# Kernel tuning notes

Hardware: AMD Instinct MI355X
Metric: run time of the kernel (lower is better)

Reference implementation:

```python
import jax, jax.numpy as jnp
import numpy as np

CHEB_K = 3


def setup_inputs() -> dict:
    key = jax.random.key(0)
    k1, k2, k3 = jax.random.split(key, 3)
    B, N, C = 64, 2048, 64
    E, O = 16, 64
    x = jax.random.normal(k1, (B, N, C), dtype=jnp.float32)
    node_embeddings = jax.random.normal(k2, (N, E), dtype=jnp.float32)
    # xavier-uniform-like init for weights_pool (embed_dim, cheb_k, dim_in, dim_out)
    fan_in, fan_out = E * CHEB_K * C, O
    limit = float(np.sqrt(6.0 / (fan_in + fan_out)))
    weights_pool = jax.random.uniform(k3, (E, CHEB_K, C, O), dtype=jnp.float32,
                                      minval=-limit, maxval=limit)
    bias_pool = jnp.zeros((E, O), dtype=jnp.float32)
    return {"x": x, "node_embeddings": node_embeddings,
            "weights_pool": weights_pool, "bias_pool": bias_pool}


def reference(x, node_embeddings, weights_pool, bias_pool):
    N = node_embeddings.shape[0]
    # adaptive adjacency: softmax(relu(E E^T)) row-wise   [N, N]
    supports = jax.nn.softmax(jax.nn.relu(node_embeddings @ node_embeddings.T), axis=1)
    # Chebyshev recurrence: T0 = I, T1 = A, Tk = 2*A*T_{k-1} - T_{k-2}
    support_set = [jnp.eye(N, dtype=supports.dtype), supports]
    for _ in range(2, CHEB_K):
        support_set.append(2.0 * supports @ support_set[-1] - support_set[-2])
    supports_k = jnp.stack(support_set, axis=0)  # [K, N, N]
    # per-node dynamic weights / bias from pools
    weights = jnp.einsum('nd,dkio->nkio', node_embeddings, weights_pool)  # [N,K,C,O]
    bias = node_embeddings @ bias_pool                                    # [N,O]
    # graph conv: gather Chebyshev features then per-node grouped GEMM
    x_g = jnp.einsum('knm,bmc->bnkc', supports_k, x)       # [B,N,K,C]
    x_gconv = jnp.einsum('bnki,nkio->bno', x_g, weights) + bias  # [B,N,O]
    return x_gconv
```

## Files before the change

kernel.cpp:

```cpp
#include <hip/hip_runtime.h>
#include <hip/hip_bf16.h>

#define BB 64
#define NN 2048
#define CC 64
#define EE 16
#define OO 64
#define JJ 4096

typedef __attribute__((ext_vector_type(8))) short short8;
typedef __attribute__((ext_vector_type(4))) float f32x4;
typedef __attribute__((ext_vector_type(4))) unsigned short u16x4;
typedef __attribute__((ext_vector_type(8))) unsigned short u16x8;

__device__ __forceinline__ unsigned short f2bf(float f) {
  __hip_bfloat16 h = __float2bfloat16(f);
  return *reinterpret_cast<unsigned short*>(&h);
}
__device__ __forceinline__ float bf2f(unsigned short u) {
  unsigned int v = ((unsigned int)u) << 16;
  return *reinterpret_cast<float*>(&v);
}
__device__ __forceinline__ void gload16(const void* g, void* l) {
  __builtin_amdgcn_global_load_lds(
      (const __attribute__((address_space(1))) unsigned int*)g,
      (__attribute__((address_space(3))) unsigned int*)l, 16, 0, 0);
}

__global__ __launch_bounds__(256) void supports_kernel(
    const float* __restrict__ emb, unsigned short* __restrict__ A)
{
  int n = blockIdx.x;
  int tid = threadIdx.x;
  float en[EE];
#pragma unroll
  for (int d = 0; d < EE; ++d) en[d] = emb[n*EE + d];

  float logit[8];
  float lmax = 0.0f;
#pragma unroll
  for (int i = 0; i < 8; ++i) {
    int m = i*256 + tid;
    const float* em = emb + m*EE;
    float s = 0.f;
#pragma unroll
    for (int d = 0; d < EE; ++d) s = fmaf(en[d], em[d], s);
    s = fmaxf(s, 0.f);
    logit[i] = s;
    lmax = fmaxf(lmax, s);
  }
  __shared__ float red[256];
  red[tid] = lmax; __syncthreads();
  for (int s = 128; s > 0; s >>= 1) {
    if (tid < s) red[tid] = fmaxf(red[tid], red[tid+s]);
    __syncthreads();
  }
  lmax = red[0]; __syncthreads();
  float sum = 0.f;
#pragma unroll
  for (int i = 0; i < 8; ++i) {
    float e = __expf(logit[i]-lmax);
    logit[i] = e; sum += e;
  }
  red[tid] = sum; __syncthreads();
  for (int s = 128; s > 0; s >>= 1) {
    if (tid < s) red[tid] += red[tid+s];
    __syncthreads();
  }
  float inv = 1.f/red[0];
#pragma unroll
  for (int i = 0; i < 8; ++i) A[(size_t)n*NN + i*256 + tid] = f2bf(logit[i]*inv);
}

__global__ __launch_bounds__(256) void xpose_kernel(
    const float* __restrict__ x, unsigned short* __restrict__ Xt)
{
  int b = blockIdx.y;
  int n0 = blockIdx.x * 64;
  __shared__ float T[64][65];
  int tid = threadIdx.x;
  int r = tid >> 4, c4 = (tid & 15) * 4;
  const float* src = x + ((size_t)b*NN + n0)*64;
#pragma unroll
  for (int rr = r; rr < 64; rr += 16) {
    float4 v = *(const float4*)(src + rr*64 + c4);
    T[rr][c4] = v.x; T[rr][c4+1] = v.y; T[rr][c4+2] = v.z; T[rr][c4+3] = v.w;
  }
  __syncthreads();
  int c = tid >> 2, q0 = (tid & 3) * 16;
  unsigned short* dst = Xt + ((size_t)b*64 + c)*NN + n0 + q0;
  u16x8 o0, o1;
#pragma unroll
  for (int q = 0; q < 8; ++q) o0[q] = f2bf(T[q0+q][c]);
#pragma unroll
  for (int q = 0; q < 8; ++q) o1[q] = f2bf(T[q0+8+q][c]);
  *(u16x8*)(dst) = o0;
  *(u16x8*)(dst + 8) = o1;
}

#define BAR() do { asm volatile("" ::: "memory"); __builtin_amdgcn_s_barrier(); \
                   asm volatile("" ::: "memory"); } while(0)

__global__ __launch_bounds__(512) void gemm_bt_8p(
    const unsigned short* __restrict__ A, const unsigned short* __restrict__ Bt,
    unsigned short* __restrict__ Crow, unsigned short* __restrict__ Ct, int writeT)
{
  __shared__ unsigned short As[3][128*64];
  __shared__ unsigned short Bs[3][256*64];
  int tid = threadIdx.x;
  int bid = blockIdx.x;
  int swz = (bid & 7) * 32 + (bid >> 3);
  int m0 = (swz >> 4) * 128, j0 = (swz & 15) * 256;
  int wid = tid >> 6, lane = tid & 63;
  int wm = wid >> 2, wn = wid & 3;
  int fr = lane & 15, kg = lane >> 4;
  int lrow = lane >> 3, lu = lane & 7;

  f32x4 acc[4][4];
#pragma unroll
  for (int i = 0; i < 4; ++i)
#pragma unroll
    for (int j = 0; j < 4; ++j) acc[i][j] = (f32x4){0.f,0.f,0.f,0.f};

  auto stageA = [&](int bW, int k0, int c) {
    int rb = wid*16 + c*8;
    gload16(A + (size_t)(m0 + rb + lrow)*2048 + k0 + (lu ^ lrow)*8, &As[bW][rb*64]);
  };
  auto stageB = [&](int bW, int k0, int c) {
    int rb = wid*32 + c*8;
    gload16(Bt + (size_t)(j0 + rb + lrow)*2048 + k0 + (lu ^ lrow)*8, &Bs[bW][rb*64]);
  };
  auto phase = [&](int bR, int q) {
    int qi = q >> 1, qj = q & 1;
    short8 af[2][2], bv[2][2];
#pragma unroll
    for (int di = 0; di < 2; ++di)
#pragma unroll
      for (int ks = 0; ks < 2; ++ks) {
        int r = wm*64 + (qi*2 + di)*16 + fr;
        int u = ((ks << 2) | kg) ^ (r & 7);
        af[di][ks] = *(const short8*)((const char*)&As[bR][0] + r*128 + u*16);
      }
#pragma unroll
    for (int dj = 0; dj < 2; ++dj)
#pragma unroll
      for (int ks = 0; ks < 2; ++ks) {
        int r = wn*64 + (qj*2 + dj)*16 + fr;
        int u = ((ks << 2) | kg) ^ (r & 7);
        bv[dj][ks] = *(const short8*)((const char*)&Bs[bR][0] + r*128 + u*16);
      }
    __builtin_amdgcn_s_setprio(1);
#pragma unroll
    for (int di = 0; di < 2; ++di)
#pragma unroll
      for (int dj = 0; dj < 2; ++dj)
#pragma unroll
        for (int ks = 0; ks < 2; ++ks)
          acc[qi*2+di][qj*2+dj] = __builtin_amdgcn_mfma_f32_16x16x32_bf16(
              af[di][ks], bv[dj][ks], acc[qi*2+di][qj*2+dj], 0, 0, 0);
    __builtin_amdgcn_s_setprio(0);
  };

#define TILE(bR, bW, kS, DOST, EW) do {                                   \
    if (DOST) { stageA(bW, kS, 0); stageB(bW, kS, 0); }                   \
    phase(bR, 0); BAR();                                                  \
    if (DOST) { stageA(bW, kS, 1); stageB(bW, kS, 1); }                   \
    phase(bR, 1); BAR();                                                  \
    if (DOST) { stageB(bW, kS, 2); stageB(bW, kS, 3); }                   \
    phase(bR, 2); BAR();                                                  \
    phase(bR, 3);                                                         \
    if ((EW) == 6) asm volatile("s_waitcnt vmcnt(6)" ::: "memory");       \
    else if ((EW) == 0) asm volatile("s_waitcnt vmcnt(0)" ::: "memory");  \
    if ((EW) >= 0) BAR();                                                 \
  } while(0)

  stageA(0, 0, 0); stageA(0, 0, 1);
  stageB(0, 0, 0); stageB(0, 0, 1); stageB(0, 0, 2); stageB(0, 0, 3);
  stageA(1, 64, 0); stageA(1, 64, 1);
  stageB(1, 64, 0); stageB(1, 64, 1); stageB(1, 64, 2); stageB(1, 64, 3);
  asm volatile("s_waitcnt vmcnt(6)" ::: "memory");
  BAR();

  for (int tg = 0; tg < 10; ++tg) {
    int kb = tg * 192;
    TILE(0, 2, kb + 128, 1, 6);
    TILE(1, 0, kb + 192, 1, 6);
    TILE(2, 1, kb + 256, 1, 6);
  }
  TILE(0, 2, 0, 0, 0);
  TILE(1, 0, 0, 0, -1);
#undef TILE

  int mrow4 = (lane >> 4) * 4;
#pragma unroll
  for (int i = 0; i < 4; ++i) {
    int mbase = m0 + wm*64 + i*16 + mrow4;
#pragma unroll
    for (int j = 0; j < 4; ++j) {
      int jcol = j0 + wn*64 + j*16 + fr;
      f32x4 v = acc[i][j];
      if (writeT) {
        u16x4 pk = { f2bf(v[0]), f2bf(v[1]), f2bf(v[2]), f2bf(v[3]) };
        *(u16x4*)(Ct + (size_t)jcol*2048 + mbase) = pk;
      }
      Crow[(size_t)(mbase+0)*4096 + jcol] = f2bf(v[0]);
      Crow[(size_t)(mbase+1)*4096 + jcol] = f2bf(v[1]);
      Crow[(size_t)(mbase+2)*4096 + jcol] = f2bf(v[2]);
      Crow[(size_t)(mbase+3)*4096 + jcol] = f2bf(v[3]);
    }
  }
}

__global__ __launch_bounds__(256) void wgen_kernel(
    const float* __restrict__ emb, const float* __restrict__ wp,
    unsigned short* __restrict__ wtg)
{
  __shared__ unsigned short Wlds[8][64*72];
  __shared__ float e_s[8][16];
  int tid = threadIdx.x;
  int g = blockIdx.x, r = blockIdx.y;
  int n0 = g*8;
  if (tid < 128) e_s[tid >> 4][tid & 15] = emb[n0*16 + tid];
  __syncthreads();
  int o = tid & 63, w = tid >> 6;
#pragma unroll 1
  for (int p = 0; p < 2; ++p) {
    int u = r*8 + p*4 + w;
    float acc[8][8];
#pragma unroll
    for (int n = 0; n < 8; ++n)
#pragma unroll
      for (int q = 0; q < 8; ++q) acc[n][q] = 0.f;
    const float* wpp = wp + u*512 + o;
#pragma unroll
    for (int d = 0; d < 16; ++d) {
      float wv[8];
#pragma unroll
      for (int q = 0; q < 8; ++q) wv[q] = wpp[d*12288 + q*64];
#pragma unroll
      for (int n = 0; n < 8; ++n) {
        float en = e_s[n][d];
#pragma unroll
        for (int q = 0; q < 8; ++q) acc[n][q] = fmaf(en, wv[q], acc[n][q]);
      }
    }
    int slot = (u & 7) ^ (o & 7);
#pragma unroll
    for (int n = 0; n < 8; ++n) {
      u16x8 pk;
#pragma unroll
      for (int q = 0; q < 8; ++q) pk[q] = f2bf(acc[n][q]);
      *(u16x8*)&Wlds[n][o*72 + slot*8] = pk;
    }
  }
  __syncthreads();
#pragma unroll
  for (int half = 0; half < 2; ++half) {
    int nd = half*4 + (tid >> 6);
    unsigned short* dst = wtg + (size_t)(n0+nd)*12288 + o*192 + r*64;
#pragma unroll
    for (int s = 0; s < 8; ++s)
      *(u16x8*)(dst + s*8) = *(const u16x8*)&Wlds[nd][o*72 + s*8];
  }
}

#define FNPB 4
__global__ __launch_bounds__(256) void final_mfma(
    const float* __restrict__ x, const float* __restrict__ emb,
    const float* __restrict__ bp, const unsigned short* __restrict__ wtg,
    const unsigned short* __restrict__ y1, const unsigned short* __restrict__ y2,
    float* __restrict__ out)
{
  __shared__ unsigned short Ws[2][12288];
  __shared__ unsigned short As[12288];
  int tid = threadIdx.x;
  int lane = tid & 63, wid = tid >> 6;
  int b = tid & 63;
  int fr = lane & 15, kg = lane >> 4;
  int o = wid*16 + fr;
  int nb = blockIdx.x * FNPB;

  float4 rx0[2][2], rx1[2][2];
  u16x8  ry1[2][2], ry2[2][2];

#pragma unroll
  for (int h = 0; h < 2; ++h) {
    int ul = wid + h*4;
    const float* xp = x + ((size_t)b*NN + nb)*64 + ul*8;
    rx0[0][h] = *(const float4*)xp;
    rx1[0][h] = *(const float4*)(xp + 4);
    ry1[0][h] = *(const u16x8*)(y1 + (size_t)nb*JJ + b*64 + ul*8);
    ry2[0][h] = *(const u16x8*)(y2 + (size_t)nb*JJ + b*64 + ul*8);
  }
#pragma unroll
  for (int t = 0; t < 6; ++t) {
    int base = wid*3072 + t*512;
    gload16(wtg + (size_t)nb*12288 + base + lane*8, &Ws[0][base]);
  }

#pragma unroll
  for (int i = 0; i < FNPB; ++i) {
    int n = nb + i;
    int cs = i & 1, ns = cs ^ 1;

#pragma unroll
    for (int h = 0; h < 2; ++h) {
      int ul = wid + h*4;
      float fx[8] = {rx0[cs][h].x, rx0[cs][h].y, rx0[cs][h].z, rx0[cs][h].w,
                     rx1[cs][h].x, rx1[cs][h].y, rx1[cs][h].z, rx1[cs][h].w};
      u16x8 v1 = ry1[cs][h], v2 = ry2[cs][h];
      u16x8 xb, t2;
#pragma unroll
      for (int q = 0; q < 8; ++q) {
        xb[q] = f2bf(fx[q]);
        t2[q] = f2bf(2.f*bf2f(v2[q]) - fx[q]);
      }
      int sw = ul ^ (b & 7);
      *(u16x8*)&As[b*192 + sw*8]      = xb;
      *(u16x8*)&As[b*192 + (8|sw)*8]  = v1;
      *(u16x8*)&As[b*192 + (16|sw)*8] = t2;
    }
    if (i + 1 < FNPB) {
#pragma unroll
      for (int h = 0; h < 2; ++h) {
        int ul = wid + h*4;
        const float* xp = x + ((size_t)b*NN + (n+1))*64 + ul*8;
        rx0[ns][h] = *(const float4*)xp;
        rx1[ns][h] = *(const float4*)(xp + 4);
        ry1[ns][h] = *(const u16x8*)(y1 + (size_t)(n+1)*JJ + b*64 + ul*8);
        ry2[ns][h] = *(const u16x8*)(y2 + (size_t)(n+1)*JJ + b*64 + ul*8);
      }
      asm volatile("s_waitcnt vmcnt(8)" ::: "memory");
    } else {
      asm volatile("s_waitcnt vmcnt(0)" ::: "memory");
    }
    asm volatile("s_waitcnt lgkmcnt(0)" ::: "memory");
    __builtin_amdgcn_s_barrier();
    asm volatile("" ::: "memory");

    float breg = 0.f;
#pragma unroll
    for (int d = 0; d < 16; ++d) breg = fmaf(emb[n*16 + d], bp[d*64 + o], breg);
    f32x4 acc[4];
#pragma unroll
    for (int k = 0; k < 4; ++k) acc[k] = (f32x4){breg, breg, breg, breg};

#pragma unroll
    for (int ks = 0; ks < 6; ++ks) {
      int u = ks*4 + kg;
      int ro = wid*16 + fr;
      int ub = (u & ~7) | ((u & 7) ^ (ro & 7));
      short8 bv = *(const short8*)&Ws[cs][ro*192 + ub*8];
#pragma unroll
      for (int k = 0; k < 4; ++k) {
        int ra = k*16 + fr;
        int ua = (u & ~7) | ((u & 7) ^ (ra & 7));
        short8 af = *(const short8*)&As[ra*192 + ua*8];
        acc[k] = __builtin_amdgcn_mfma_f32_16x16x32_bf16(af, bv, acc[k], 0, 0, 0);
      }
    }
    int mrow = (lane >> 4) * 4;
#pragma unroll
    for (int k = 0; k < 4; ++k) {
#pragma unroll
      for (int rr = 0; rr < 4; ++rr) {
        int brow = k*16 + mrow + rr;
        out[((size_t)brow*NN + n)*64 + o] = acc[k][rr];
      }
    }
    if (i + 1 < FNPB) {
#pragma unroll
      for (int t = 0; t < 6; ++t) {
        int base = wid*3072 + t*512;
        gload16(wtg + (size_t)(n+1)*12288 + base + lane*8, &Ws[ns][base]);
      }
    }
    asm volatile("" ::: "memory");
    __builtin_amdgcn_s_barrier();
  }
}

extern "C" void kernel_launch(void* const* d_in, const int* in_sizes, int n_in,
                              void* d_out, int out_size, void* d_ws, size_t ws_size,
                              hipStream_t stream) {
  const float* x   = (const float*)d_in[0];
  const float* emb = (const float*)d_in[1];
  const float* wp  = (const float*)d_in[2];
  const float* bp  = (const float*)d_in[3];
  float* out = (float*)d_out;

  unsigned short* Ab  = (unsigned short*)d_ws;
  unsigned short* Y1b = Ab  + (size_t)NN*NN;
  unsigned short* Y2b = Y1b + (size_t)NN*JJ;
  unsigned short* region = Y2b + (size_t)NN*JJ;
  unsigned short* Xt  = region;
  unsigned short* Y1T = region + (size_t)JJ*NN;
  unsigned short* Wtg = region;

  supports_kernel<<<NN, 256, 0, stream>>>(emb, Ab);
  xpose_kernel<<<dim3(32, 64), 256, 0, stream>>>(x, Xt);
  gemm_bt_8p<<<256, 512, 0, stream>>>(Ab, Xt,  Y1b, Y1T, 1);
  gemm_bt_8p<<<256, 512, 0, stream>>>(Ab, Y1T, Y2b, nullptr, 0);
  wgen_kernel<<<dim3(256, 3), 256, 0, stream>>>(emb, wp, Wtg);
  final_mfma<<<NN/FNPB, 256, 0, stream>>>(x, emb, bp, Wtg, Y1b, Y2b, out);
}
```

Measured before the change: 209.6 us.

## Restructure GEMM main loop into two k-split phases with interleaved async staging

Each 64-wide K tile is now processed in two phases, one per 32-wide k-slice. Each phase loads a full 4x4 fragment set from LDS, issues the global-to-LDS prefetch for the next buffer, then runs 16 MFMAs behind a barrier and sched_barrier fences. This replaces four quadrant phases with three barriers by two phases with fewer barriers and larger MFMA bursts. It lowers synchronization overhead, but raises register pressure from holding 8 fragments and changes how LDS reads and global loads overlap.

```diff
diff --git a/kernel.cpp b/kernel.cpp
--- a/kernel.cpp
+++ b/kernel.cpp
@@ -130,45 +130,39 @@
     int rb = wid*32 + c*8;
     gload16(Bt + (size_t)(j0 + rb + lrow)*2048 + k0 + (lu ^ lrow)*8, &Bs[bW][rb*64]);
   };
-  auto phase = [&](int bR, int q) {
-    int qi = q >> 1, qj = q & 1;
-    short8 af[2][2], bv[2][2];
-#pragma unroll
-    for (int di = 0; di < 2; ++di)
-#pragma unroll
-      for (int ks = 0; ks < 2; ++ks) {
-        int r = wm*64 + (qi*2 + di)*16 + fr;
-        int u = ((ks << 2) | kg) ^ (r & 7);
-        af[di][ks] = *(const short8*)((const char*)&As[bR][0] + r*128 + u*16);
-      }
-#pragma unroll
-    for (int dj = 0; dj < 2; ++dj)
-#pragma unroll
-      for (int ks = 0; ks < 2; ++ks) {
-        int r = wn*64 + (qj*2 + dj)*16 + fr;
-        int u = ((ks << 2) | kg) ^ (r & 7);
-        bv[dj][ks] = *(const short8*)((const char*)&Bs[bR][0] + r*128 + u*16);
-      }
+  auto phase = [&](int bR, int ks, int bW, int kS, int part) {
+    short8 af[4], bv[4];
+#pragma unroll
+    for (int i = 0; i < 4; ++i) {
+      int r = wm*64 + i*16 + fr;
+      int u = ((ks << 2) | kg) ^ (r & 7);
+      af[i] = *(const short8*)((const char*)&As[bR][0] + r*128 + u*16);
+    }
+#pragma unroll
+    for (int j = 0; j < 4; ++j) {
+      int r = wn*64 + j*16 + fr;
+      int u = ((ks << 2) | kg) ^ (r & 7);
+      bv[j] = *(const short8*)((const char*)&Bs[bR][0] + r*128 + u*16);
+    }
+    if (part == 0) { stageA(bW, kS, 0); stageB(bW, kS, 0); stageB(bW, kS, 1); }
+    else if (part == 1) { stageA(bW, kS, 1); stageB(bW, kS, 2); stageB(bW, kS, 3); }
+    __builtin_amdgcn_s_barrier();
+    asm volatile("s_waitcnt lgkmcnt(0)" ::: "memory");
+    __builtin_amdgcn_sched_barrier(0);
     __builtin_amdgcn_s_setprio(1);
 #pragma unroll
-    for (int di = 0; di < 2; ++di)
-#pragma unroll
-      for (int dj = 0; dj < 2; ++dj)
-#pragma unroll
-        for (int ks = 0; ks < 2; ++ks)
-          acc[qi*2+di][qj*2+dj] = __builtin_amdgcn_mfma_f32_16x16x32_bf16(
-              af[di][ks], bv[dj][ks], acc[qi*2+di][qj*2+dj], 0, 0, 0);
+    for (int i = 0; i < 4; ++i)
+#pragma unroll
+      for (int j = 0; j < 4; ++j)
+        acc[i][j] = __builtin_amdgcn_mfma_f32_16x16x32_bf16(af[i], bv[j], acc[i][j], 0, 0, 0);
     __builtin_amdgcn_s_setprio(0);
+    __builtin_amdgcn_sched_barrier(0);
   };
 
 #define TILE(bR, bW, kS, DOST, EW) do {                                   \
-    if (DOST) { stageA(bW, kS, 0); stageB(bW, kS, 0); }                   \
-    phase(bR, 0); BAR();                                                  \
-    if (DOST) { stageA(bW, kS, 1); stageB(bW, kS, 1); }                   \
-    phase(bR, 1); BAR();                                                  \
-    if (DOST) { stageB(bW, kS, 2); stageB(bW, kS, 3); }                   \
-    phase(bR, 2); BAR();                                                  \
-    phase(bR, 3);                                                         \
+    phase(bR, 0, bW, kS, (DOST) ? 0 : -1);                                \
+    BAR();                                                                \
+    phase(bR, 1, bW, kS, (DOST) ? 1 : -1);                                \
     if ((EW) == 6) asm volatile("s_waitcnt vmcnt(6)" ::: "memory");       \
     else if ((EW) == 0) asm volatile("s_waitcnt vmcnt(0)" ::: "memory");  \
     if ((EW) >= 0) BAR();                                                 \
```

Result: faster. 184.2 us (-12.1%).
